# Performance work log

Hardware: AMD Instinct MI355X
Metric: run time of the kernel (lower is better)

## Reference

```python
import jax, jax.numpy as jnp
import numpy as np

H = 16          # num_heads
MAX_SCALE_MUL = float(np.log(100.0))
EPS = 1e-12     # F.normalize eps


def setup_inputs() -> dict:
    key = jax.random.key(0)
    ks = jax.random.split(key, 8)
    B, L, C = 8, 1024, 1024
    x = jax.random.normal(ks[0], (B, L, C), dtype=jnp.float32)
    attn_bias = jax.random.normal(ks[1], (1, H, L, L), dtype=jnp.float32) * 0.1
    w_qkv = jax.random.normal(ks[2], (3 * C, C), dtype=jnp.float32) * (C ** -0.5)
    q_bias = jnp.zeros((C,), dtype=jnp.float32)
    v_bias = jnp.zeros((C,), dtype=jnp.float32)
    scale_mul = jnp.full((1, H, 1, 1), np.log(4.0), dtype=jnp.float32)
    w_proj = jax.random.normal(ks[3], (C, C), dtype=jnp.float32) * (C ** -0.5)
    b_proj = jnp.zeros((C,), dtype=jnp.float32)
    return dict(x=x, attn_bias=attn_bias, w_qkv=w_qkv, q_bias=q_bias,
                v_bias=v_bias, scale_mul=scale_mul, w_proj=w_proj, b_proj=b_proj)


def _l2norm(t):
    # matches F.normalize(dim=-1): t / max(||t||_2, eps)
    n = jnp.sqrt(jnp.sum(t * t, axis=-1, keepdims=True))
    return t / jnp.maximum(n, EPS)


def reference(x, attn_bias, w_qkv, q_bias, v_bias, scale_mul, w_proj, b_proj):
    B, L, C = x.shape
    D = C // H
    bias = jnp.concatenate([q_bias, jnp.zeros_like(q_bias), v_bias])
    qkv = x @ w_qkv.T + bias                      # [B,L,3C]
    qkv = qkv.reshape(B, L, 3, H, D).transpose(2, 0, 3, 1, 4)  # [3,B,H,L,D]
    q, k, v = qkv[0], qkv[1], qkv[2]
    sm = jnp.exp(jnp.minimum(scale_mul, MAX_SCALE_MUL))        # [1,H,1,1]
    q = _l2norm(q) * sm
    k = _l2norm(k)
    attn = jnp.einsum('bhld,bhmd->bhlm', q, k) + attn_bias     # scale == 1
    attn = jax.nn.softmax(attn, axis=-1)
    out = jnp.einsum('bhlm,bhmd->bhld', attn, v)               # [B,H,L,D]
    out = out.transpose(0, 2, 1, 3).reshape(B, L, C)
    return out @ w_proj.T + b_proj
```

## Files before the change

kernel.cpp:

```cpp
#include <hip/hip_runtime.h>


#define LN100 4.6051701859880914f

typedef __attribute__((ext_vector_type(8))) short short8;
typedef __attribute__((ext_vector_type(4))) float f32x4;

#define MFMA_BF16(a, b, c) __builtin_amdgcn_mfma_f32_16x16x32_bf16(a, b, c, 0, 0, 0)

__device__ __forceinline__ unsigned short f2bf(float f) {
  unsigned u = __float_as_uint(f);
  u += 0x7fffu + ((u >> 16) & 1u);
  return (unsigned short)(u >> 16);
}
__device__ __forceinline__ float bf2f(unsigned short h) {
  return __uint_as_float(((unsigned)h) << 16);
}

__device__ __forceinline__ float bias_sel0(const float* qb, const float* vb, int col) {
  if (col < 1024) return qb[col];
  if (col < 2048) return 0.0f;
  return vb[col - 2048];
}

#define G2L16(gp, lp) __builtin_amdgcn_global_load_lds( \
    (const __attribute__((address_space(1))) void*)(gp), \
    (__attribute__((address_space(3))) void*)(lp), 16, 0, 0)

__global__ __launch_bounds__(256)
void split_f32_bf16(const float* __restrict__ in, unsigned short* __restrict__ hi,
                    unsigned short* __restrict__ lo, int n4)
{
  int i = blockIdx.x * blockDim.x + threadIdx.x;
  if (i >= n4) return;
  float4 v = ((const float4*)in)[i];
  ushort4 h, l;
  h.x = f2bf(v.x); l.x = f2bf(v.x - bf2f(h.x));
  h.y = f2bf(v.y); l.y = f2bf(v.y - bf2f(h.y));
  h.z = f2bf(v.z); l.z = f2bf(v.z - bf2f(h.z));
  h.w = f2bf(v.w); l.w = f2bf(v.w - bf2f(h.w));
  ((ushort4*)hi)[i] = h;
  ((ushort4*)lo)[i] = l;
}

template <int MODE>
__global__ __launch_bounds__(256)
void gemm_nt_split(const unsigned short* __restrict__ Ah, const unsigned short* __restrict__ Al,
                   const unsigned short* __restrict__ Wh, const unsigned short* __restrict__ Wl,
                   const float* __restrict__ b0, const float* __restrict__ b1,
                   float* __restrict__ C,
                   unsigned short* __restrict__ vth, unsigned short* __restrict__ vtl,
                   int M, int N, int K)
{
  __shared__ unsigned short sA[128 * 64];
  __shared__ unsigned short sW[128 * 64];

  const int tid  = threadIdx.x;
  const int lane = tid & 63;
  const int l15  = lane & 15, lg = lane >> 4;
  const int w    = tid >> 6;
  const int wr   = (w >> 1) << 6;
  const int wc   = (w & 1) << 6;
  const int m0   = blockIdx.y << 7;
  const int n0   = blockIdx.x << 7;

  f32x4 acc[4][4];
  #pragma unroll
  for (int i = 0; i < 4; ++i)
    #pragma unroll
    for (int j = 0; j < 4; ++j)
      acc[i][j] = (f32x4){0.f, 0.f, 0.f, 0.f};

  for (int k0 = 0; k0 < K; k0 += 32) {
    __syncthreads();
    #pragma unroll
    for (int u = 0; u < 4; ++u) {
      int idx = (u << 8) + tid;
      int row = idx >> 3;
      int c   = idx & 7;
      int s   = c ^ (row & 7);
      size_t rbA = (size_t)(m0 + row) * K + k0;
      size_t rbW = (size_t)(n0 + row) * K + k0;
      const unsigned short* srcA = (s < 4) ? (Ah + rbA + (s << 3))
                                           : (Al + rbA + ((s - 4) << 3));
      const unsigned short* srcW = (s < 4) ? (Wh + rbW + (s << 3))
                                           : (Wl + rbW + ((s - 4) << 3));
      G2L16(srcA, sA + (idx << 3));
      G2L16(srcW, sW + (idx << 3));
    }
    __syncthreads();

    short8 ah[4], al[4];
    #pragma unroll
    for (int i = 0; i < 4; ++i) {
      int row = wr + (i << 4) + l15;
      ah[i] = *(const short8*)(sA + (row << 6) + ((lg       ^ (row & 7)) << 3));
      al[i] = *(const short8*)(sA + (row << 6) + (((4 + lg) ^ (row & 7)) << 3));
    }
    #pragma unroll
    for (int j = 0; j < 4; ++j) {
      int row = wc + (j << 4) + l15;
      short8 wh = *(const short8*)(sW + (row << 6) + ((lg       ^ (row & 7)) << 3));
      short8 wl = *(const short8*)(sW + (row << 6) + (((4 + lg) ^ (row & 7)) << 3));
      #pragma unroll
      for (int i = 0; i < 4; ++i) {
        acc[i][j] = MFMA_BF16(ah[i], wh, acc[i][j]);
        acc[i][j] = MFMA_BF16(ah[i], wl, acc[i][j]);
        acc[i][j] = MFMA_BF16(al[i], wh, acc[i][j]);
      }
    }
  }

  if (MODE == 0 && n0 >= 2048) {
    #pragma unroll
    for (int j = 0; j < 4; ++j) {
      int col = n0 + wc + (j << 4) + l15;
      int d   = col - 2048;
      int hh  = d >> 6, dd = d & 63;
      float bb = b1[d];
      #pragma unroll
      for (int i = 0; i < 4; ++i) {
        int row  = m0 + wr + (i << 4) + (lg << 2);
        int bidx = row >> 10;
        int l    = row & 1023;
        size_t obase = ((((size_t)bidx << 4) + hh) << 6) + dd;
        obase = obase * 1024 + l;
        ushort4 hv, lv;
        float v0 = acc[i][j][0] + bb;
        float v1 = acc[i][j][1] + bb;
        float v2 = acc[i][j][2] + bb;
        float v3 = acc[i][j][3] + bb;
        hv.x = f2bf(v0); lv.x = f2bf(v0 - bf2f(hv.x));
        hv.y = f2bf(v1); lv.y = f2bf(v1 - bf2f(hv.y));
        hv.z = f2bf(v2); lv.z = f2bf(v2 - bf2f(hv.z));
        hv.w = f2bf(v3); lv.w = f2bf(v3 - bf2f(hv.w));
        *(ushort4*)(vth + obase) = hv;
        *(ushort4*)(vtl + obase) = lv;
      }
    }
  } else {
    #pragma unroll
    for (int j = 0; j < 4; ++j) {
      int col = n0 + wc + (j << 4) + l15;
      float bb = (MODE == 1) ? b0[col] : bias_sel0(b0, b1, col);
      #pragma unroll
      for (int i = 0; i < 4; ++i) {
        int rbase = m0 + wr + (i << 4) + (lg << 2);
        #pragma unroll
        for (int r = 0; r < 4; ++r)
          C[(size_t)(rbase + r) * N + col] = acc[i][j][r] + bb;
      }
    }
  }
}

__global__ __launch_bounds__(256)
void qk_norm_split(const float* __restrict__ qkv, const float* __restrict__ scale_mul,
                   unsigned short* __restrict__ qk_h, unsigned short* __restrict__ qk_l)
{
  int wave = (blockIdx.x << 2) + (threadIdx.x >> 6);
  int lane = threadIdx.x & 63;
  int h  = wave & 15;
  int bl = wave >> 4;
  size_t base = (size_t)bl * 3072 + (h << 6) + lane;
  float q = qkv[base];
  float k = qkv[base + 1024];
  float sq = q * q, sk = k * k;
  #pragma unroll
  for (int off = 32; off; off >>= 1) {
    sq += __shfl_xor(sq, off);
    sk += __shfl_xor(sk, off);
  }
  float sm = __expf(fminf(scale_mul[h], LN100));
  q = q / fmaxf(sqrtf(sq), 1e-12f) * sm;
  k = k / fmaxf(sqrtf(sk), 1e-12f);
  size_t ob = (size_t)bl * 2048 + (h << 6) + lane;
  unsigned short qh = f2bf(q);
  qk_h[ob] = qh;          qk_l[ob] = f2bf(q - bf2f(qh));
  unsigned short kh = f2bf(k);
  qk_h[ob + 1024] = kh;   qk_l[ob + 1024] = f2bf(k - bf2f(kh));
}

__global__ __launch_bounds__(256, 2)
void attn_mfma(const unsigned short* __restrict__ qk_h, const unsigned short* __restrict__ qk_l,
               const unsigned short* __restrict__ vth, const unsigned short* __restrict__ vtl,
               const float* __restrict__ bias,
               unsigned short* __restrict__ oh, unsigned short* __restrict__ ol)
{
  __shared__ unsigned short sKh[4096], sKl[4096];
  __shared__ unsigned short sVh[4096], sVl[4096];
  __shared__ unsigned short sPh[8192], sPl[8192];

  const int tid  = threadIdx.x;
  const int lane = tid & 63;
  const int l15  = lane & 15, lg = lane >> 4;
  const int w    = tid >> 6;
  const int qt = blockIdx.x & 7;
  const int h  = (blockIdx.x >> 3) & 15;
  const int b  = blockIdx.x >> 7;
  const int q0 = qt << 7;

  short8 qh[2][2], qlo[2][2];
  #pragma unroll
  for (int qf = 0; qf < 2; ++qf) {
    size_t rb = ((size_t)((b << 10) + q0 + (w << 5) + (qf << 4) + l15)) * 2048
              + (h << 6) + (lg << 3);
    qh[qf][0]  = *(const short8*)(qk_h + rb);
    qh[qf][1]  = *(const short8*)(qk_h + rb + 32);
    qlo[qf][0] = *(const short8*)(qk_l + rb);
    qlo[qf][1] = *(const short8*)(qk_l + rb + 32);
  }

  f32x4 ao[2][4];
  float mr[2][4], lr[2][4];
  #pragma unroll
  for (int qf = 0; qf < 2; ++qf) {
    #pragma unroll
    for (int j = 0; j < 4; ++j) ao[qf][j] = (f32x4){0.f, 0.f, 0.f, 0.f};
    #pragma unroll
    for (int r = 0; r < 4; ++r) { mr[qf][r] = -3.0e38f; lr[qf][r] = 0.0f; }
  }

  const unsigned short* kh_base = qk_h + 1024 + (h << 6);
  const unsigned short* kl_base = qk_l + 1024 + (h << 6);
  const size_t vbase = ((size_t)((b << 4) + h)) * 65536;

  for (int kv0 = 0; kv0 < 1024; kv0 += 64) {
    __syncthreads();
    #pragma unroll
    for (int u = 0; u < 2; ++u) {
      int idx = (u << 8) + tid;
      int r = idx >> 3, c = idx & 7;
      int s = c ^ (r & 7);
      size_t krow = (size_t)((b << 10) + kv0 + r) * 2048 + (s << 3);
      size_t vrow = vbase + (size_t)r * 1024 + kv0 + (s << 3);
      G2L16(kh_base + krow, sKh + (idx << 3));
      G2L16(kl_base + krow, sKl + (idx << 3));
      G2L16(vth + vrow,     sVh + (idx << 3));
      G2L16(vtl + vrow,     sVl + (idx << 3));
    }
    float bb[2][4][4];
    #pragma unroll
    for (int qf = 0; qf < 2; ++qf)
      #pragma unroll
      for (int r = 0; r < 4; ++r) {
        int qrow = q0 + (w << 5) + (qf << 4) + (lg << 2) + r;
        const float* bp = bias + ((size_t)h << 20) + (size_t)qrow * 1024 + kv0 + l15;
        #pragma unroll
        for (int j = 0; j < 4; ++j) bb[qf][r][j] = bp[j << 4];
      }
    __syncthreads();

    f32x4 sv[2][4];
    #pragma unroll
    for (int j = 0; j < 4; ++j) {
      f32x4 a0 = (f32x4){0.f, 0.f, 0.f, 0.f};
      f32x4 a1 = (f32x4){0.f, 0.f, 0.f, 0.f};
      #pragma unroll
      for (int ks = 0; ks < 2; ++ks) {
        int row = (j << 4) + l15;
        int c   = (lg + (ks << 2)) ^ (row & 7);
        short8 kh = *(const short8*)(sKh + (row << 6) + (c << 3));
        short8 kl = *(const short8*)(sKl + (row << 6) + (c << 3));
        a0 = MFMA_BF16(qh[0][ks], kh, a0);
        a0 = MFMA_BF16(qh[0][ks], kl, a0);
        a0 = MFMA_BF16(qlo[0][ks], kh, a0);
        a1 = MFMA_BF16(qh[1][ks], kh, a1);
        a1 = MFMA_BF16(qh[1][ks], kl, a1);
        a1 = MFMA_BF16(qlo[1][ks], kh, a1);
      }
      sv[0][j] = a0;
      sv[1][j] = a1;
    }

    #pragma unroll
    for (int qf = 0; qf < 2; ++qf) {
      float p[4][4], alpha[4];
      #pragma unroll
      for (int r = 0; r < 4; ++r) {
        float s0 = sv[qf][0][r] + bb[qf][r][0];
        float s1 = sv[qf][1][r] + bb[qf][r][1];
        float s2 = sv[qf][2][r] + bb[qf][r][2];
        float s3 = sv[qf][3][r] + bb[qf][r][3];
        float mx = fmaxf(fmaxf(s0, s1), fmaxf(s2, s3));
        #pragma unroll
        for (int o = 1; o < 16; o <<= 1) mx = fmaxf(mx, __shfl_xor(mx, o));
        float mn = fmaxf(mr[qf][r], mx);
        alpha[r] = __expf(mr[qf][r] - mn);
        p[r][0] = __expf(s0 - mn); p[r][1] = __expf(s1 - mn);
        p[r][2] = __expf(s2 - mn); p[r][3] = __expf(s3 - mn);
        float rs = p[r][0] + p[r][1] + p[r][2] + p[r][3];
        #pragma unroll
        for (int o = 1; o < 16; o <<= 1) rs += __shfl_xor(rs, o);
        lr[qf][r] = lr[qf][r] * alpha[r] + rs;
        mr[qf][r] = mn;
      }
      #pragma unroll
      for (int jd = 0; jd < 4; ++jd)
        #pragma unroll
        for (int r = 0; r < 4; ++r)
          ao[qf][jd][r] *= alpha[r];
      #pragma unroll
      for (int r = 0; r < 4; ++r) {
        int q2 = (w << 5) + (qf << 4) + (lg << 2) + r;
        #pragma unroll
        for (int j = 0; j < 4; ++j) {
          unsigned short hb = f2bf(p[r][j]);
          unsigned short lb = f2bf(p[r][j] - bf2f(hb));
          int c = ((j << 1) + (l15 >> 3)) ^ (q2 & 7);
          int e = (q2 << 6) + (c << 3) + (l15 & 7);
          sPh[e] = hb;
          sPl[e] = lb;
        }
      }
    }

    #pragma unroll
    for (int ks = 0; ks < 2; ++ks) {
      short8 ph[2], pl[2];
      #pragma unroll
      for (int qf = 0; qf < 2; ++qf) {
        int prow = (w << 5) + (qf << 4) + l15;
        int pc   = (lg + (ks << 2)) ^ (prow & 7);
        ph[qf] = *(const short8*)(sPh + (prow << 6) + (pc << 3));
        pl[qf] = *(const short8*)(sPl + (prow << 6) + (pc << 3));
      }
      #pragma unroll
      for (int jd = 0; jd < 4; ++jd) {
        int vrow = (jd << 4) + l15;
        int vc   = (lg + (ks << 2)) ^ (vrow & 7);
        short8 vh = *(const short8*)(sVh + (vrow << 6) + (vc << 3));
        short8 vl = *(const short8*)(sVl + (vrow << 6) + (vc << 3));
        #pragma unroll
        for (int qf = 0; qf < 2; ++qf) {
          ao[qf][jd] = MFMA_BF16(ph[qf], vh, ao[qf][jd]);
          ao[qf][jd] = MFMA_BF16(ph[qf], vl, ao[qf][jd]);
          ao[qf][jd] = MFMA_BF16(pl[qf], vh, ao[qf][jd]);
        }
      }
    }
  }

  #pragma unroll
  for (int qf = 0; qf < 2; ++qf)
    #pragma unroll
    for (int r = 0; r < 4; ++r) {
      float inv = 1.0f / lr[qf][r];
      size_t orow = ((size_t)((b << 10) + q0 + (w << 5) + (qf << 4) + (lg << 2) + r)) * 1024
                  + (h << 6) + l15;
      #pragma unroll
      for (int jd = 0; jd < 4; ++jd) {
        float v = ao[qf][jd][r] * inv;
        unsigned short hb = f2bf(v);
        oh[orow + (jd << 4)] = hb;
        ol[orow + (jd << 4)] = f2bf(v - bf2f(hb));
      }
    }
}

template <int MODE>
__global__ __launch_bounds__(256)
void gemm_nt(const float* __restrict__ A, const float* __restrict__ Bw,
             const float* __restrict__ b0, const float* __restrict__ b1,
             float* __restrict__ C, int M, int N, int K)
{
  __shared__ float As[32][132];
  __shared__ float Bs[32][132];
  const int tid = threadIdx.x;
  const int tx = tid & 15, ty = tid >> 4;
  const int m0 = blockIdx.y << 7;
  const int n0 = blockIdx.x << 7;

  float acc[8][8];
  #pragma unroll
  for (int i = 0; i < 8; ++i)
    #pragma unroll
    for (int j = 0; j < 8; ++j) acc[i][j] = 0.0f;

  for (int k0 = 0; k0 < K; k0 += 32) {
    #pragma unroll
    for (int u = 0; u < 4; ++u) {
      int f   = tid + (u << 8);
      int row = f >> 3;
      int kk  = (f & 7) << 2;
      float4 av = *(const float4*)(A  + (size_t)(m0 + row) * K + k0 + kk);
      As[kk + 0][row] = av.x; As[kk + 1][row] = av.y;
      As[kk + 2][row] = av.z; As[kk + 3][row] = av.w;
      float4 bv = *(const float4*)(Bw + (size_t)(n0 + row) * K + k0 + kk);
      Bs[kk + 0][row] = bv.x; Bs[kk + 1][row] = bv.y;
      Bs[kk + 2][row] = bv.z; Bs[kk + 3][row] = bv.w;
    }
    __syncthreads();
    #pragma unroll
    for (int kk = 0; kk < 32; ++kk) {
      float a[8], b[8];
      *(float4*)(a)     = *(const float4*)(&As[kk][(ty << 3)]);
      *(float4*)(a + 4) = *(const float4*)(&As[kk][(ty << 3) + 4]);
      *(float4*)(b)     = *(const float4*)(&Bs[kk][(tx << 3)]);
      *(float4*)(b + 4) = *(const float4*)(&Bs[kk][(tx << 3) + 4]);
      #pragma unroll
      for (int i = 0; i < 8; ++i)
        #pragma unroll
        for (int j = 0; j < 8; ++j)
          acc[i][j] = fmaf(a[i], b[j], acc[i][j]);
    }
    __syncthreads();
  }

  #pragma unroll
  for (int i = 0; i < 8; ++i) {
    int row = m0 + (ty << 3) + i;
    #pragma unroll
    for (int j4 = 0; j4 < 2; ++j4) {
      int col = n0 + (tx << 3) + (j4 << 2);
      float4 r;
      float bb[4];
      #pragma unroll
      for (int j = 0; j < 4; ++j)
        bb[j] = (MODE == 0) ? bias_sel0(b0, b1, col + j) : b0[col + j];
      r.x = acc[i][j4 * 4 + 0] + bb[0];
      r.y = acc[i][j4 * 4 + 1] + bb[1];
      r.z = acc[i][j4 * 4 + 2] + bb[2];
      r.w = acc[i][j4 * 4 + 3] + bb[3];
      *(float4*)(C + (size_t)row * N + col) = r;
    }
  }
}

__global__ __launch_bounds__(256)
void qk_norm(float* __restrict__ qkv, const float* __restrict__ scale_mul)
{
  int wave = (blockIdx.x << 2) + (threadIdx.x >> 6);
  int lane = threadIdx.x & 63;
  int h  = wave & 15;
  int bl = wave >> 4;
  size_t base = (size_t)bl * 3072 + (h << 6) + lane;
  float q = qkv[base];
  float k = qkv[base + 1024];
  float sq = q * q, sk = k * k;
  #pragma unroll
  for (int off = 32; off; off >>= 1) {
    sq += __shfl_xor(sq, off);
    sk += __shfl_xor(sk, off);
  }
  float sm = __expf(fminf(scale_mul[h], LN100));
  q = q / fmaxf(sqrtf(sq), 1e-12f) * sm;
  k = k / fmaxf(sqrtf(sk), 1e-12f);
  qkv[base]        = q;
  qkv[base + 1024] = k;
}

#define SW(r, c4) ((((c4) ^ ((r) >> 2)) & 15) << 2)

template <int OUTMODE>
__global__ __launch_bounds__(256)
void attn_fwd(const float* __restrict__ qkv, const float* __restrict__ bias,
              float* __restrict__ aout,
              unsigned short* __restrict__ ah, unsigned short* __restrict__ al)
{
  __shared__ float Qs[64][64];
  __shared__ float Ks[64][64];
  __shared__ float Vs[64][64];
  __shared__ float Ps[64][64];

  const int tid = threadIdx.x;
  const int tx = tid & 15, ty = tid >> 4;
  const int qt = blockIdx.x & 15;
  const int h  = (blockIdx.x >> 4) & 15;
  const int b  = blockIdx.x >> 8;
  const int q0 = qt << 6;

  #pragma unroll
  for (int u = 0; u < 4; ++u) {
    int f = tid + (u << 8);
    int r = f >> 4, c4 = f & 15;
    float4 v = *(const float4*)(qkv + (size_t)(b * 1024 + q0 + r) * 3072 + (h << 6) + (c4 << 2));
    *(float4*)(&Qs[r][SW(r, c4)]) = v;
  }

  float o[4][4];
  float mr[4], lr[4];
  #pragma unroll
  for (int i = 0; i < 4; ++i) {
    mr[i] = -3.0e38f; lr[i] = 0.0f;
    #pragma unroll
    for (int j = 0; j < 4; ++j) o[i][j] = 0.0f;
  }

  for (int kv0 = 0; kv0 < 1024; kv0 += 64) {
    __syncthreads();
    #pragma unroll
    for (int u = 0; u < 4; ++u) {
      int f = tid + (u << 8);
      int r = f >> 4, c4 = f & 15;
      size_t gb = (size_t)(b * 1024 + kv0 + r) * 3072 + (h << 6) + (c4 << 2);
      *(float4*)(&Ks[r][SW(r, c4)]) = *(const float4*)(qkv + gb + 1024);
      *(float4*)(&Vs[r][SW(r, c4)]) = *(const float4*)(qkv + gb + 2048);
    }
    __syncthreads();

    float s[4][4];
    #pragma unroll
    for (int i = 0; i < 4; ++i)
      #pragma unroll
      for (int j = 0; j < 4; ++j) s[i][j] = 0.0f;

    #pragma unroll 4
    for (int d4 = 0; d4 < 16; ++d4) {
      float4 qv[4], kv[4];
      #pragma unroll
      for (int i = 0; i < 4; ++i)
        qv[i] = *(const float4*)(&Qs[(ty << 2) + i][SW((ty << 2) + i, d4)]);
      #pragma unroll
      for (int j = 0; j < 4; ++j)
        kv[j] = *(const float4*)(&Ks[(tx << 2) + j][SW((tx << 2) + j, d4)]);
      #pragma unroll
      for (int i = 0; i < 4; ++i)
        #pragma unroll
        for (int j = 0; j < 4; ++j)
          s[i][j] += qv[i].x * kv[j].x + qv[i].y * kv[j].y +
                     qv[i].z * kv[j].z + qv[i].w * kv[j].w;
    }

    float p[4][4];
    #pragma unroll
    for (int i = 0; i < 4; ++i) {
      float4 bv = *(const float4*)(bias + (size_t)((h << 10) + q0 + (ty << 2) + i) * 1024
                                        + kv0 + (tx << 2));
      s[i][0] += bv.x; s[i][1] += bv.y; s[i][2] += bv.z; s[i][3] += bv.w;
      float mx = fmaxf(fmaxf(s[i][0], s[i][1]), fmaxf(s[i][2], s[i][3]));
      #pragma unroll
      for (int off = 1; off < 16; off <<= 1) mx = fmaxf(mx, __shfl_xor(mx, off));
      float mn = fmaxf(mr[i], mx);
      float alp = __expf(mr[i] - mn);
      float rs = 0.0f;
      #pragma unroll
      for (int j = 0; j < 4; ++j) { p[i][j] = __expf(s[i][j] - mn); rs += p[i][j]; }
      #pragma unroll
      for (int off = 1; off < 16; off <<= 1) rs += __shfl_xor(rs, off);
      lr[i] = lr[i] * alp + rs;
      mr[i] = mn;
      #pragma unroll
      for (int j = 0; j < 4; ++j) o[i][j] *= alp;
    }

    #pragma unroll
    for (int jj = 0; jj < 4; ++jj)
      #pragma unroll
      for (int i = 0; i < 4; ++i)
        Ps[(tx << 2) + jj][SW((tx << 2) + jj, ty) + i] = p[i][jj];
    __syncthreads();

    #pragma unroll 8
    for (int j = 0; j < 64; ++j) {
      float4 pv = *(const float4*)(&Ps[j][SW(j, ty)]);
      float4 vv = *(const float4*)(&Vs[j][SW(j, tx)]);
      o[0][0] += pv.x * vv.x; o[0][1] += pv.x * vv.y; o[0][2] += pv.x * vv.z; o[0][3] += pv.x * vv.w;
      o[1][0] += pv.y * vv.x; o[1][1] += pv.y * vv.y; o[1][2] += pv.y * vv.z; o[1][3] += pv.y * vv.w;
      o[2][0] += pv.z * vv.x; o[2][1] += pv.z * vv.y; o[2][2] += pv.z * vv.z; o[2][3] += pv.z * vv.w;
      o[3][0] += pv.w * vv.x; o[3][1] += pv.w * vv.y; o[3][2] += pv.w * vv.z; o[3][3] += pv.w * vv.w;
    }
  }

  #pragma unroll
  for (int i = 0; i < 4; ++i) {
    float inv = 1.0f / lr[i];
    float v0 = o[i][0] * inv, v1 = o[i][1] * inv, v2 = o[i][2] * inv, v3 = o[i][3] * inv;
    if (OUTMODE == 0) {
      float4 r; r.x = v0; r.y = v1; r.z = v2; r.w = v3;
      *(float4*)(aout + (size_t)(b * 1024 + q0 + (ty << 2) + i) * 1024 + (h << 6) + (tx << 2)) = r;
    } else {
      ushort4 hh, ll;
      hh.x = f2bf(v0); ll.x = f2bf(v0 - bf2f(hh.x));
      hh.y = f2bf(v1); ll.y = f2bf(v1 - bf2f(hh.y));
      hh.z = f2bf(v2); ll.z = f2bf(v2 - bf2f(hh.z));
      hh.w = f2bf(v3); ll.w = f2bf(v3 - bf2f(hh.w));
      size_t idx = (size_t)(b * 1024 + q0 + (ty << 2) + i) * 256 + (h << 4) + tx;
      ((ushort4*)ah)[idx] = hh;
      ((ushort4*)al)[idx] = ll;
    }
  }
}

extern "C" void kernel_launch(void* const* d_in, const int* in_sizes, int n_in,
                              void* d_out, int out_size, void* d_ws, size_t ws_size,
                              hipStream_t stream) {
  const float* x         = (const float*)d_in[0];
  const float* attn_bias = (const float*)d_in[1];
  const float* w_qkv     = (const float*)d_in[2];
  const float* q_bias    = (const float*)d_in[3];
  const float* v_bias    = (const float*)d_in[4];
  const float* scale_mul = (const float*)d_in[5];
  const float* w_proj    = (const float*)d_in[6];
  const float* b_proj    = (const float*)d_in[7];
  float* out = (float*)d_out;

  const size_t MiB = 1024 * 1024;
  char* ws = (char*)d_ws;
  dim3 blk(256);

  if (ws_size >= 240 * MiB) {
    float*          qkv = (float*)ws;
    unsigned short* xh  = (unsigned short*)(ws + 96  * MiB);
    unsigned short* xl  = (unsigned short*)(ws + 112 * MiB);
    unsigned short* qkh = (unsigned short*)(ws + 128 * MiB);
    unsigned short* qkl = (unsigned short*)(ws + 160 * MiB);
    unsigned short* vth = (unsigned short*)(ws + 192 * MiB);
    unsigned short* vtl = (unsigned short*)(ws + 208 * MiB);
    unsigned short* wqh = (unsigned short*)(ws + 224 * MiB);
    unsigned short* wql = (unsigned short*)(ws + 230 * MiB);
    unsigned short* wph = (unsigned short*)(ws + 236 * MiB);
    unsigned short* wpl = (unsigned short*)(ws + 238 * MiB);

    split_f32_bf16<<<dim3(8192), blk, 0, stream>>>(x,      xh,  xl,  2097152);
    split_f32_bf16<<<dim3(3072), blk, 0, stream>>>(w_qkv,  wqh, wql, 786432);
    split_f32_bf16<<<dim3(1024), blk, 0, stream>>>(w_proj, wph, wpl, 262144);

    gemm_nt_split<0><<<dim3(24, 64), blk, 0, stream>>>(xh, xl, wqh, wql,
        q_bias, v_bias, qkv, vth, vtl, 8192, 3072, 1024);
    qk_norm_split<<<dim3(32768), blk, 0, stream>>>(qkv, scale_mul, qkh, qkl);
    attn_mfma<<<dim3(1024), blk, 0, stream>>>(qkh, qkl, vth, vtl, attn_bias, xh, xl);
    gemm_nt_split<1><<<dim3(8, 64), blk, 0, stream>>>(xh, xl, wph, wpl,
        b_proj, nullptr, out, nullptr, nullptr, 8192, 1024, 1024);
  } else if (ws_size >= 144 * MiB) {
    float*          qkv = (float*)ws;
    unsigned short* xh  = (unsigned short*)(ws + 96  * MiB);
    unsigned short* xl  = (unsigned short*)(ws + 112 * MiB);
    unsigned short* wqh = (unsigned short*)(ws + 128 * MiB);
    unsigned short* wql = (unsigned short*)(ws + 134 * MiB);
    unsigned short* wph = (unsigned short*)(ws + 140 * MiB);
    unsigned short* wpl = (unsigned short*)(ws + 142 * MiB);

    split_f32_bf16<<<dim3(8192), blk, 0, stream>>>(x,      xh,  xl,  2097152);
    split_f32_bf16<<<dim3(3072), blk, 0, stream>>>(w_qkv,  wqh, wql, 786432);
    split_f32_bf16<<<dim3(1024), blk, 0, stream>>>(w_proj, wph, wpl, 262144);

    gemm_nt_split<2><<<dim3(24, 64), blk, 0, stream>>>(xh, xl, wqh, wql,
        q_bias, v_bias, qkv, nullptr, nullptr, 8192, 3072, 1024);
    qk_norm<<<dim3(32768), blk, 0, stream>>>(qkv, scale_mul);
    attn_fwd<1><<<dim3(2048), blk, 0, stream>>>(qkv, attn_bias, nullptr, xh, xl);
    gemm_nt_split<1><<<dim3(8, 64), blk, 0, stream>>>(xh, xl, wph, wpl,
        b_proj, nullptr, out, nullptr, nullptr, 8192, 1024, 1024);
  } else {
    float* qkv = (float*)ws;
    float* att = qkv + (size_t)8192 * 3072;
    gemm_nt<0><<<dim3(24, 64), blk, 0, stream>>>(x, w_qkv, q_bias, v_bias, qkv, 8192, 3072, 1024);
    qk_norm<<<dim3(32768), blk, 0, stream>>>(qkv, scale_mul);
    attn_fwd<0><<<dim3(2048), blk, 0, stream>>>(qkv, attn_bias, att, nullptr, nullptr);
    gemm_nt<1><<<dim3(8, 64), blk, 0, stream>>>(att, w_proj, b_proj, nullptr, out, 8192, 1024, 1024);
  }
}
```

Before: 602.3 us.

## Compute transposed S in attention so P stays in registers, dropping LDS round-trip

The QK^T MFMA now swaps operands to produce S^T, so each lane holds one query row's scores across four keys. Softmax row statistics then need only two cross-lane shuffles instead of four. The P fragments are packed to bf16 hi/lo in registers and fed straight to the PV MFMA. This removes the sP shared-memory buffers, their scattered stores and their reloads. In exchange, V is now read from LDS as split 8-byte halves, alpha and l need per-row shuffles, and the bias is loaded as float4.

```diff
diff --git a/kernel.cpp b/kernel.cpp
--- a/kernel.cpp
+++ b/kernel.cpp
@@ -1,9 +1,11 @@
 #include <hip/hip_runtime.h>
+#include <hip/hip_bf16.h>
 
 
 #define LN100 4.6051701859880914f
 
 typedef __attribute__((ext_vector_type(8))) short short8;
+typedef __attribute__((ext_vector_type(4))) short short4v;
 typedef __attribute__((ext_vector_type(4))) float f32x4;
 
 #define MFMA_BF16(a, b, c) __builtin_amdgcn_mfma_f32_16x16x32_bf16(a, b, c, 0, 0, 0)
@@ -15,6 +17,11 @@
 }
 __device__ __forceinline__ float bf2f(unsigned short h) {
   return __uint_as_float(((unsigned)h) << 16);
+}
+__device__ __forceinline__ unsigned int pkbf2(float a, float b) {
+  union { __hip_bfloat162 t; unsigned int u; } c;
+  c.t = __float22bfloat162_rn(make_float2(a, b));
+  return c.u;
 }
 
 __device__ __forceinline__ float bias_sel0(const float* qb, const float* vb, int col) {
@@ -189,7 +196,6 @@
 {
   __shared__ unsigned short sKh[4096], sKl[4096];
   __shared__ unsigned short sVh[4096], sVl[4096];
-  __shared__ unsigned short sPh[8192], sPl[8192];
 
   const int tid  = threadIdx.x;
   const int lane = tid & 63;
@@ -212,18 +218,19 @@
   }
 
   f32x4 ao[2][4];
-  float mr[2][4], lr[2][4];
+  float mr[2], lr[2];
   #pragma unroll
   for (int qf = 0; qf < 2; ++qf) {
     #pragma unroll
     for (int j = 0; j < 4; ++j) ao[qf][j] = (f32x4){0.f, 0.f, 0.f, 0.f};
-    #pragma unroll
-    for (int r = 0; r < 4; ++r) { mr[qf][r] = -3.0e38f; lr[qf][r] = 0.0f; }
+    mr[qf] = -3.0e38f; lr[qf] = 0.0f;
   }
 
   const unsigned short* kh_base = qk_h + 1024 + (h << 6);
   const unsigned short* kl_base = qk_l + 1024 + (h << 6);
   const size_t vbase = ((size_t)((b << 4) + h)) * 65536;
+  const float* bias_base = bias + ((size_t)h << 20)
+                         + (size_t)(q0 + (w << 5) + l15) * 1024 + (lg << 2);
 
   for (int kv0 = 0; kv0 < 1024; kv0 += 64) {
     __syncthreads();
@@ -239,104 +246,118 @@
       G2L16(vth + vrow,     sVh + (idx << 3));
       G2L16(vtl + vrow,     sVl + (idx << 3));
     }
-    float bb[2][4][4];
+    float4 bb[2][4];
     #pragma unroll
     for (int qf = 0; qf < 2; ++qf)
       #pragma unroll
+      for (int j = 0; j < 4; ++j)
+        bb[qf][j] = *(const float4*)(bias_base + (size_t)(qf << 4) * 1024
+                                     + kv0 + (j << 4));
+    __syncthreads();
+
+    f32x4 sv[2][4];
+    #pragma unroll
+    for (int j = 0; j < 4; ++j) {
+      int row = (j << 4) + l15;
+      int c0 = lg ^ (row & 7);
+      int c1 = (lg + 4) ^ (row & 7);
+      short8 kh0 = *(const short8*)(sKh + (row << 6) + (c0 << 3));
+      short8 kl0 = *(const short8*)(sKl + (row << 6) + (c0 << 3));
+      short8 kh1 = *(const short8*)(sKh + (row << 6) + (c1 << 3));
+      short8 kl1 = *(const short8*)(sKl + (row << 6) + (c1 << 3));
+      #pragma unroll
+      for (int qf = 0; qf < 2; ++qf) {
+        f32x4 a = (f32x4){0.f, 0.f, 0.f, 0.f};
+        a = MFMA_BF16(kh0, qh[qf][0], a);
+        a = MFMA_BF16(kl0, qh[qf][0], a);
+        a = MFMA_BF16(kh0, qlo[qf][0], a);
+        a = MFMA_BF16(kh1, qh[qf][1], a);
+        a = MFMA_BF16(kl1, qh[qf][1], a);
+        a = MFMA_BF16(kh1, qlo[qf][1], a);
+        sv[qf][j] = a;
+      }
+    }
+
+    unsigned int phw[2][8], plw[2][8];
+    #pragma unroll
+    for (int qf = 0; qf < 2; ++qf) {
+      #pragma unroll
+      for (int j = 0; j < 4; ++j) {
+        sv[qf][j][0] += bb[qf][j].x;
+        sv[qf][j][1] += bb[qf][j].y;
+        sv[qf][j][2] += bb[qf][j].z;
+        sv[qf][j][3] += bb[qf][j].w;
+      }
+      float mx = -3.0e38f;
+      #pragma unroll
+      for (int j = 0; j < 4; ++j)
+        #pragma unroll
+        for (int r = 0; r < 4; ++r) mx = fmaxf(mx, sv[qf][j][r]);
+      mx = fmaxf(mx, __shfl_xor(mx, 16));
+      mx = fmaxf(mx, __shfl_xor(mx, 32));
+      float mn = fmaxf(mr[qf], mx);
+      float al = __expf(mr[qf] - mn);
+      mr[qf] = mn;
+      float rs = 0.0f;
+      #pragma unroll
+      for (int j = 0; j < 4; ++j)
+        #pragma unroll
+        for (int r = 0; r < 4; ++r) {
+          float e = __expf(sv[qf][j][r] - mn);
+          sv[qf][j][r] = e;
+          rs += e;
+        }
+      rs += __shfl_xor(rs, 16);
+      rs += __shfl_xor(rs, 32);
+      lr[qf] = lr[qf] * al + rs;
+      #pragma unroll
       for (int r = 0; r < 4; ++r) {
-        int qrow = q0 + (w << 5) + (qf << 4) + (lg << 2) + r;
-        const float* bp = bias + ((size_t)h << 20) + (size_t)qrow * 1024 + kv0 + l15;
+        float av = __shfl(al, (lg << 2) + r);
         #pragma unroll
-        for (int j = 0; j < 4; ++j) bb[qf][r][j] = bp[j << 4];
-      }
-    __syncthreads();
-
-    f32x4 sv[2][4];
-    #pragma unroll
-    for (int j = 0; j < 4; ++j) {
-      f32x4 a0 = (f32x4){0.f, 0.f, 0.f, 0.f};
-      f32x4 a1 = (f32x4){0.f, 0.f, 0.f, 0.f};
-      #pragma unroll
-      for (int ks = 0; ks < 2; ++ks) {
-        int row = (j << 4) + l15;
-        int c   = (lg + (ks << 2)) ^ (row & 7);
-        short8 kh = *(const short8*)(sKh + (row << 6) + (c << 3));
-        short8 kl = *(const short8*)(sKl + (row << 6) + (c << 3));
-        a0 = MFMA_BF16(qh[0][ks], kh, a0);
-        a0 = MFMA_BF16(qh[0][ks], kl, a0);
-        a0 = MFMA_BF16(qlo[0][ks], kh, a0);
-        a1 = MFMA_BF16(qh[1][ks], kh, a1);
-        a1 = MFMA_BF16(qh[1][ks], kl, a1);
-        a1 = MFMA_BF16(qlo[1][ks], kh, a1);
-      }
-      sv[0][j] = a0;
-      sv[1][j] = a1;
-    }
-
-    #pragma unroll
-    for (int qf = 0; qf < 2; ++qf) {
-      float p[4][4], alpha[4];
-      #pragma unroll
-      for (int r = 0; r < 4; ++r) {
-        float s0 = sv[qf][0][r] + bb[qf][r][0];
-        float s1 = sv[qf][1][r] + bb[qf][r][1];
-        float s2 = sv[qf][2][r] + bb[qf][r][2];
-        float s3 = sv[qf][3][r] + bb[qf][r][3];
-        float mx = fmaxf(fmaxf(s0, s1), fmaxf(s2, s3));
-        #pragma unroll
-        for (int o = 1; o < 16; o <<= 1) mx = fmaxf(mx, __shfl_xor(mx, o));
-        float mn = fmaxf(mr[qf][r], mx);
-        alpha[r] = __expf(mr[qf][r] - mn);
-        p[r][0] = __expf(s0 - mn); p[r][1] = __expf(s1 - mn);
-        p[r][2] = __expf(s2 - mn); p[r][3] = __expf(s3 - mn);
-        float rs = p[r][0] + p[r][1] + p[r][2] + p[r][3];
-        #pragma unroll
-        for (int o = 1; o < 16; o <<= 1) rs += __shfl_xor(rs, o);
-        lr[qf][r] = lr[qf][r] * alpha[r] + rs;
-        mr[qf][r] = mn;
-      }
-      #pragma unroll
-      for (int jd = 0; jd < 4; ++jd)
-        #pragma unroll
-        for (int r = 0; r < 4; ++r)
-          ao[qf][jd][r] *= alpha[r];
-      #pragma unroll
-      for (int r = 0; r < 4; ++r) {
-        int q2 = (w << 5) + (qf << 4) + (lg << 2) + r;
-        #pragma unroll
-        for (int j = 0; j < 4; ++j) {
-          unsigned short hb = f2bf(p[r][j]);
-          unsigned short lb = f2bf(p[r][j] - bf2f(hb));
-          int c = ((j << 1) + (l15 >> 3)) ^ (q2 & 7);
-          int e = (q2 << 6) + (c << 3) + (l15 & 7);
-          sPh[e] = hb;
-          sPl[e] = lb;
-        }
+        for (int jd = 0; jd < 4; ++jd) ao[qf][jd][r] *= av;
+      }
+      #pragma unroll
+      for (int j = 0; j < 4; ++j) {
+        unsigned int h0 = pkbf2(sv[qf][j][0], sv[qf][j][1]);
+        unsigned int h1 = pkbf2(sv[qf][j][2], sv[qf][j][3]);
+        float r0 = sv[qf][j][0] - __uint_as_float(h0 << 16);
+        float r1 = sv[qf][j][1] - __uint_as_float(h0 & 0xffff0000u);
+        float r2 = sv[qf][j][2] - __uint_as_float(h1 << 16);
+        float r3 = sv[qf][j][3] - __uint_as_float(h1 & 0xffff0000u);
+        phw[qf][(j << 1)]     = h0;
+        phw[qf][(j << 1) + 1] = h1;
+        plw[qf][(j << 1)]     = pkbf2(r0, r1);
+        plw[qf][(j << 1) + 1] = pkbf2(r2, r3);
       }
     }
 
     #pragma unroll
     for (int ks = 0; ks < 2; ++ks) {
-      short8 ph[2], pl[2];
-      #pragma unroll
-      for (int qf = 0; qf < 2; ++qf) {
-        int prow = (w << 5) + (qf << 4) + l15;
-        int pc   = (lg + (ks << 2)) ^ (prow & 7);
-        ph[qf] = *(const short8*)(sPh + (prow << 6) + (pc << 3));
-        pl[qf] = *(const short8*)(sPl + (prow << 6) + (pc << 3));
+      union { unsigned int w[4]; short8 v; } pa0, pa1, pl0, pl1;
+      #pragma unroll
+      for (int i = 0; i < 4; ++i) {
+        pa0.w[i] = phw[0][(ks << 2) + i];
+        pa1.w[i] = phw[1][(ks << 2) + i];
+        pl0.w[i] = plw[0][(ks << 2) + i];
+        pl1.w[i] = plw[1][(ks << 2) + i];
       }
       #pragma unroll
       for (int jd = 0; jd < 4; ++jd) {
-        int vrow = (jd << 4) + l15;
-        int vc   = (lg + (ks << 2)) ^ (vrow & 7);
-        short8 vh = *(const short8*)(sVh + (vrow << 6) + (vc << 3));
-        short8 vl = *(const short8*)(sVl + (vrow << 6) + (vc << 3));
-        #pragma unroll
-        for (int qf = 0; qf < 2; ++qf) {
-          ao[qf][jd] = MFMA_BF16(ph[qf], vh, ao[qf][jd]);
-          ao[qf][jd] = MFMA_BF16(ph[qf], vl, ao[qf][jd]);
-          ao[qf][jd] = MFMA_BF16(pl[qf], vh, ao[qf][jd]);
-        }
+        int vr  = (jd << 4) + l15;
+        int c0  = ((ks << 2) + (lg >> 1))     ^ (vr & 7);
+        int c1  = ((ks << 2) + 2 + (lg >> 1)) ^ (vr & 7);
+        int sub = (lg & 1) << 2;
+        short8 vh, vl;
+        vh.lo = *(const short4v*)(sVh + (vr << 6) + (c0 << 3) + sub);
+        vh.hi = *(const short4v*)(sVh + (vr << 6) + (c1 << 3) + sub);
+        vl.lo = *(const short4v*)(sVl + (vr << 6) + (c0 << 3) + sub);
+        vl.hi = *(const short4v*)(sVl + (vr << 6) + (c1 << 3) + sub);
+        ao[0][jd] = MFMA_BF16(pa0.v, vh, ao[0][jd]);
+        ao[0][jd] = MFMA_BF16(pa0.v, vl, ao[0][jd]);
+        ao[0][jd] = MFMA_BF16(pl0.v, vh, ao[0][jd]);
+        ao[1][jd] = MFMA_BF16(pa1.v, vh, ao[1][jd]);
+        ao[1][jd] = MFMA_BF16(pa1.v, vl, ao[1][jd]);
+        ao[1][jd] = MFMA_BF16(pl1.v, vh, ao[1][jd]);
       }
     }
   }
@@ -345,7 +366,8 @@
   for (int qf = 0; qf < 2; ++qf)
     #pragma unroll
     for (int r = 0; r < 4; ++r) {
-      float inv = 1.0f / lr[qf][r];
+      float lv  = __shfl(lr[qf], (lg << 2) + r);
+      float inv = 1.0f / lv;
       size_t orow = ((size_t)((b << 10) + q0 + (w << 5) + (qf << 4) + (lg << 2) + r)) * 1024
                   + (h << 6) + l15;
       #pragma unroll
@@ -393,16 +415,16 @@
     __syncthreads();
     #pragma unroll
     for (int kk = 0; kk < 32; ++kk) {
-      float a[8], b[8];
-      *(float4*)(a)     = *(const float4*)(&As[kk][(ty << 3)]);
-      *(float4*)(a + 4) = *(const float4*)(&As[kk][(ty << 3) + 4]);
-      *(float4*)(b)     = *(const float4*)(&Bs[kk][(tx << 3)]);
-      *(float4*)(b + 4) = *(const float4*)(&Bs[kk][(tx << 3) + 4]);
+      float a[8], bq[8];
+      *(float4*)(a)      = *(const float4*)(&As[kk][(ty << 3)]);
+      *(float4*)(a + 4)  = *(const float4*)(&As[kk][(ty << 3) + 4]);
+      *(float4*)(bq)     = *(const float4*)(&Bs[kk][(tx << 3)]);
+      *(float4*)(bq + 4) = *(const float4*)(&Bs[kk][(tx << 3) + 4]);
       #pragma unroll
       for (int i = 0; i < 8; ++i)
         #pragma unroll
         for (int j = 0; j < 8; ++j)
-          acc[i][j] = fmaf(a[i], b[j], acc[i][j]);
+          acc[i][j] = fmaf(a[i], bq[j], acc[i][j]);
     }
     __syncthreads();
   }
@@ -414,14 +436,14 @@
     for (int j4 = 0; j4 < 2; ++j4) {
       int col = n0 + (tx << 3) + (j4 << 2);
       float4 r;
-      float bb[4];
+      float bbv[4];
       #pragma unroll
       for (int j = 0; j < 4; ++j)
-        bb[j] = (MODE == 0) ? bias_sel0(b0, b1, col + j) : b0[col + j];
-      r.x = acc[i][j4 * 4 + 0] + bb[0];
-      r.y = acc[i][j4 * 4 + 1] + bb[1];
-      r.z = acc[i][j4 * 4 + 2] + bb[2];
-      r.w = acc[i][j4 * 4 + 3] + bb[3];
+        bbv[j] = (MODE == 0) ? bias_sel0(b0, b1, col + j) : b0[col + j];
+      r.x = acc[i][j4 * 4 + 0] + bbv[0];
+      r.y = acc[i][j4 * 4 + 1] + bbv[1];
+      r.z = acc[i][j4 * 4 + 2] + bbv[2];
+      r.w = acc[i][j4 * 4 + 3] + bbv[3];
       *(float4*)(C + (size_t)row * N + col) = r;
     }
   }
```

After: 540.9 us. 1.11x faster.
